# Kernel tuning notes

Hardware: AMD Instinct MI355X
Metric: run time of the kernel (lower is better)

Reference implementation:

```python
import jax, jax.numpy as jnp
import numpy as np

N = 8192      # nodes
NIN = 128     # input feature dim
NH = 128      # hidden dim
NC = 8        # communities
CS = N // NC  # community size


def setup_inputs() -> dict:
    key = jax.random.key(0)
    k = jax.random.split(key, 6)
    seq1 = jax.random.normal(k[0], (1, N, NIN), jnp.float32)
    seq2 = jax.random.normal(k[1], (1, N, NIN), jnp.float32)
    # dense row-stochastic-ish adjacency so GCN activations stay O(1)
    adj = jax.random.uniform(k[2], (1, N, N), jnp.float32) * (2.0 / N)
    cc_label = jnp.arange(N, dtype=jnp.int32).reshape(NC, CS)  # partition of nodes
    W = jax.random.normal(k[3], (NIN, NH), jnp.float32) / np.float32(np.sqrt(NIN))
    b = jnp.zeros((NH,), jnp.float32)
    Wb = jax.random.normal(k[4], (NH, NH), jnp.float32) / np.float32(np.sqrt(NH))
    bb = jnp.zeros((), jnp.float32)
    return {"seq1": seq1, "seq2": seq2, "adj": adj, "cc_label": cc_label,
            "W": W, "b": b, "Wb": Wb, "bb": bb}


def reference(seq1, seq2, adj, cc_label, W, b, Wb, bb):
    def gcn(seq):
        fts = jnp.einsum('bnd,dh->bnh', seq, W)            # linear
        agg = jnp.einsum('bnm,bmh->bnh', adj, fts) + b     # neighborhood aggregation
        return jax.nn.relu(agg)

    h1 = gcn(seq1)[0]   # [N, NH]
    h2 = gcn(seq2)[0]   # [N, NH]

    # ragged per-community gather (communities are equal-size here)
    hg1 = h1[cc_label]  # [NC, CS, NH]
    hg2 = h2[cc_label]  # [NC, CS, NH]

    # AvgReadout (msk=None) + sigmoid -> per-community summary
    c = jax.nn.sigmoid(jnp.mean(hg1, axis=1))              # [NC, NH]

    # Discriminator: bilinear f_k(h, c) = h @ Wb @ c + bb
    cw = jnp.einsum('hk,nk->nh', Wb, c)                    # [NC, NH]
    sc1 = jnp.einsum('nch,nh->nc', hg1, cw) + bb           # [NC, CS]
    sc2 = jnp.einsum('nch,nh->nc', hg2, cw) + bb           # [NC, CS]

    # scalar scatter-back (each node written exactly once)
    flat = cc_label.reshape(-1)
    ret1 = jnp.zeros((N,), h1.dtype).at[flat].set(sc1.reshape(-1))
    ret2 = jnp.zeros((N,), h2.dtype).at[flat].set(sc2.reshape(-1))
    return jnp.concatenate([ret1, ret2])[None, :]          # [1, 2N]
```

## Files before the change

kernel.cpp:

```cpp
#include <hip/hip_runtime.h>


#define NN    8192
#define NCOLS 256
#define ASCALE 4096.0f
#define AINV  (1.0f/4096.0f)

typedef _Float16 half8 __attribute__((ext_vector_type(8)));
typedef float    f32x4 __attribute__((ext_vector_type(4)));

__device__ __forceinline__ void gload16(const void* g, void* l) {
  __builtin_amdgcn_global_load_lds(
      (const __attribute__((address_space(1))) char*)g,
      (__attribute__((address_space(3))) char*)l, 16, 0, 0);
}

__global__ void k0_init(const int* __restrict__ cc, int* __restrict__ node_comm,
                        float* __restrict__ S) {
  int i = blockIdx.x * 256 + threadIdx.x;
  if (i < 1024) S[i] = 0.0f;
  node_comm[cc[i]] = i >> 10;
}

__global__ __launch_bounds__(256) void k1_fts(const float* __restrict__ seq1,
                                              const float* __restrict__ seq2,
                                              const float* __restrict__ W,
                                              _Float16* __restrict__ F) {
  __shared__ char lds[65536];
  _Float16* Wt  = (_Float16*)lds;
  float*    sSeq = (float*)(lds + 32768);
  const int tid = threadIdx.x;
  const int lane = tid & 63;
  const int w = tid >> 6;
  const int l15 = lane & 15;
  const int g = lane >> 4;
  const int m0 = blockIdx.x * 64;

  for (int it = 0; it < 64; ++it) {
    int idx = it * 256 + tid;
    int d = idx >> 7, hc = idx & 127;
    int byte = (hc * 256 + d * 2) ^ ((hc & 7) << 4);
    *(_Float16*)(lds + byte) = (_Float16)W[idx];
  }

  const float* seqp[2] = {seq1, seq2};
  const int srow = tid >> 5;
  const int sck = tid & 31;

  for (int s = 0; s < 2; ++s) {
    __syncthreads();
    const float* sp = seqp[s];
#pragma unroll
    for (int i = 0; i < 8; ++i) {
      int row = i * 8 + srow;
      gload16(sp + (size_t)(m0 + row) * 128 + ((sck ^ (row & 7)) << 2),
              (char*)sSeq + i * 4096 + w * 1024);
    }
    asm volatile("s_waitcnt vmcnt(0)" ::: "memory");
    __syncthreads();

    f32x4 acc[4][2] = {};
    const float4* S4 = (const float4*)sSeq;
    const float4* W4 = (const float4*)Wt;
#pragma unroll
    for (int kk = 0; kk < 4; ++kk) {
      half8 bf[2];
#pragma unroll
      for (int nf = 0; nf < 2; ++nf) {
        int col = w * 32 + nf * 16 + l15;
        float4 bv = W4[(col * 16 + kk * 4 + g) ^ (col & 7)];
        bf[nf] = *(const half8*)&bv;
      }
#pragma unroll
      for (int mf = 0; mf < 4; ++mf) {
        int row = mf * 16 + l15;
        int bidx = row * 32 + kk * 8 + g * 2;
        float4 u = S4[bidx ^ (row & 7)];
        float4 v = S4[(bidx + 1) ^ (row & 7)];
        half8 af;
#pragma unroll
        for (int j = 0; j < 4; ++j) af[j] = (_Float16)(((const float*)&u)[j]);
#pragma unroll
        for (int j = 0; j < 4; ++j) af[4 + j] = (_Float16)(((const float*)&v)[j]);
#pragma unroll
        for (int nf = 0; nf < 2; ++nf)
          acc[mf][nf] = __builtin_amdgcn_mfma_f32_16x16x32_f16(af, bf[nf], acc[mf][nf], 0, 0, 0);
      }
    }
    __syncthreads();
    _Float16* img = (_Float16*)sSeq;
#pragma unroll
    for (int mf = 0; mf < 4; ++mf)
#pragma unroll
      for (int nf = 0; nf < 2; ++nf) {
        int col = w * 32 + nf * 16 + l15;
#pragma unroll
        for (int j = 0; j < 4; ++j) {
          int kl = mf * 16 + g * 4 + j;
          img[(kl >> 5) * 4096 + col * 32 + (kl & 31)] = (_Float16)acc[mf][nf][j];
        }
      }
    __syncthreads();
    const float4* src4 = (const float4*)sSeq;
#pragma unroll
    for (int i = 0; i < 4; ++i) {
      int e = i * 256 + tid;
      int kt = e >> 9, off = e & 511;
      ((float4*)(F + (size_t)(2 * blockIdx.x + kt) * 8192))[s * 512 + off] = src4[e];
    }
  }
}

__global__ __launch_bounds__(512) void k2_gemm(const float* __restrict__ adj,
                                               const _Float16* __restrict__ F,
                                               float* __restrict__ Pp) {
  __shared__ float    sA0[4096];
  __shared__ float    sA1[4096];
  __shared__ _Float16 sB0[8192];
  __shared__ _Float16 sB1[8192];
  const int tid = threadIdx.x;
  const int lane = tid & 63;
  const int w = tid >> 6;
  const int l15 = lane & 15;
  const int g = lane >> 4;
  const int row0 = blockIdx.x * 128;
  const int ks = blockIdx.y;
  const int kcol0 = ks * 2048;

  const int ar0 = tid >> 3;
  const int ac = tid & 7;
  const float* asrc0 = adj + (size_t)(row0 + ar0) * NN + kcol0 + ((ac ^ (ar0 & 7)) << 2);
  const float* asrc1 = adj + (size_t)(row0 + ar0 + 64) * NN + kcol0 + ((ac ^ (ar0 & 7)) << 2);
  const char*  bsrc  = (const char*)F + (size_t)(ks * 64) * 16384 + (size_t)tid * 16;

  auto stage = [&](float* sA, _Float16* sB, int t) {
    gload16(asrc0 + t * 32, (char*)sA + w * 1024);
    gload16(asrc1 + t * 32, (char*)sA + 8192 + w * 1024);
    const char* bs = bsrc + (size_t)t * 16384;
    gload16(bs,        (char*)sB + w * 1024);
    gload16(bs + 8192, (char*)sB + 8192 + w * 1024);
  };

  const int wm = w >> 2, wn = w & 3;
  f32x4 acc[4][4] = {};

  auto compute = [&](const float* sA, const _Float16* sB) {
    const float4* A4 = (const float4*)sA;
    const float4* B4 = (const float4*)sB;
    half8 bf[4];
#pragma unroll
    for (int nf = 0; nf < 4; ++nf) {
      int col = wn * 64 + nf * 16 + l15;
      float4 bv = B4[col * 4 + g];
      bf[nf] = *(const half8*)&bv;
    }
#pragma unroll
    for (int mf = 0; mf < 4; ++mf) {
      int row = wm * 64 + mf * 16 + l15;
      int bidx = row * 8 + g * 2;
      float4 u = A4[bidx ^ (row & 7)];
      float4 v = A4[(bidx + 1) ^ (row & 7)];
      half8 af;
#pragma unroll
      for (int j = 0; j < 4; ++j) af[j] = (_Float16)(((const float*)&u)[j] * ASCALE);
#pragma unroll
      for (int j = 0; j < 4; ++j) af[4 + j] = (_Float16)(((const float*)&v)[j] * ASCALE);
#pragma unroll
      for (int nf = 0; nf < 4; ++nf)
        acc[mf][nf] = __builtin_amdgcn_mfma_f32_16x16x32_f16(af, bf[nf], acc[mf][nf], 0, 0, 0);
    }
  };

  stage(sA0, sB0, 0);
  asm volatile("s_waitcnt vmcnt(0)" ::: "memory");
  __syncthreads();
  for (int t = 0; t < 64; t += 2) {
    stage(sA1, sB1, t + 1);
    compute(sA0, sB0);
    asm volatile("s_waitcnt vmcnt(0)" ::: "memory");
    __syncthreads();
    if (t + 2 < 64) stage(sA0, sB0, t + 2);
    compute(sA1, sB1);
    asm volatile("s_waitcnt vmcnt(0)" ::: "memory");
    __syncthreads();
  }

#pragma unroll
  for (int mf = 0; mf < 4; ++mf)
#pragma unroll
    for (int nf = 0; nf < 4; ++nf) {
      int col = wn * 64 + nf * 16 + l15;
#pragma unroll
      for (int j = 0; j < 4; ++j) {
        int row = row0 + wm * 64 + mf * 16 + g * 4 + j;
        Pp[((size_t)ks * NN + row) * NCOLS + col] = acc[mf][nf][j];
      }
    }
}

__global__ void k2r_reduce(const float* __restrict__ Pp, const float* __restrict__ b,
                           float* __restrict__ h) {
  int gid = blockIdx.x * 256 + threadIdx.x;
  size_t base = (size_t)gid * 4;
  float4 p0 = *(const float4*)(Pp + base);
  float4 p1 = *(const float4*)(Pp + base + 2097152);
  float4 p2 = *(const float4*)(Pp + base + 4194304);
  float4 p3 = *(const float4*)(Pp + base + 6291456);
  int n0 = (int)(base & 255) & 127;
  float4 r;
  r.x = fmaxf((p0.x + p1.x + p2.x + p3.x) * AINV + b[n0],     0.f);
  r.y = fmaxf((p0.y + p1.y + p2.y + p3.y) * AINV + b[n0 + 1], 0.f);
  r.z = fmaxf((p0.z + p1.z + p2.z + p3.z) * AINV + b[n0 + 2], 0.f);
  r.w = fmaxf((p0.w + p1.w + p2.w + p3.w) * AINV + b[n0 + 3], 0.f);
  *(float4*)(h + base) = r;
}

__global__ __launch_bounds__(128) void k3a_csum(const float* __restrict__ h,
                                                const int* __restrict__ node_comm,
                                                float* __restrict__ S) {
  int hh = threadIdx.x;
  int n0 = blockIdx.x * 32;
  float a0=0,a1=0,a2=0,a3=0,a4=0,a5=0,a6=0,a7=0;
  for (int i = 0; i < 32; ++i) {
    int node = n0 + i;
    int c = node_comm[node];
    float v = h[(size_t)node * 256 + hh];
    a0 += (c == 0) ? v : 0.f;  a1 += (c == 1) ? v : 0.f;
    a2 += (c == 2) ? v : 0.f;  a3 += (c == 3) ? v : 0.f;
    a4 += (c == 4) ? v : 0.f;  a5 += (c == 5) ? v : 0.f;
    a6 += (c == 6) ? v : 0.f;  a7 += (c == 7) ? v : 0.f;
  }
  if (a0 != 0.f) atomicAdd(&S[0 * 128 + hh], a0);
  if (a1 != 0.f) atomicAdd(&S[1 * 128 + hh], a1);
  if (a2 != 0.f) atomicAdd(&S[2 * 128 + hh], a2);
  if (a3 != 0.f) atomicAdd(&S[3 * 128 + hh], a3);
  if (a4 != 0.f) atomicAdd(&S[4 * 128 + hh], a4);
  if (a5 != 0.f) atomicAdd(&S[5 * 128 + hh], a5);
  if (a6 != 0.f) atomicAdd(&S[6 * 128 + hh], a6);
  if (a7 != 0.f) atomicAdd(&S[7 * 128 + hh], a7);
}

__global__ __launch_bounds__(128) void k3b_cw(const float* __restrict__ S,
                                              const float* __restrict__ Wb,
                                              float* __restrict__ cw) {
  __shared__ float sc[128];
  int ci = blockIdx.x;
  int hh = threadIdx.x;
  float m = S[ci * 128 + hh] * (1.0f / 1024.0f);
  sc[hh] = 1.0f / (1.0f + __expf(-m));
  __syncthreads();
  const float4* wr = (const float4*)(Wb + (size_t)hh * 128);
  float acc = 0.f;
#pragma unroll 8
  for (int k4 = 0; k4 < 32; ++k4) {
    float4 wv = wr[k4];
    acc += wv.x * sc[k4 * 4 + 0] + wv.y * sc[k4 * 4 + 1]
         + wv.z * sc[k4 * 4 + 2] + wv.w * sc[k4 * 4 + 3];
  }
  cw[ci * 128 + hh] = acc;
}

__global__ __launch_bounds__(256) void k5_score(const float* __restrict__ h,
                                                const int* __restrict__ node_comm,
                                                const float* __restrict__ cw,
                                                const float* __restrict__ bbp,
                                                float* __restrict__ out) {
  int tid = threadIdx.x;
  int q = tid & 15, nl = tid >> 4;
  int node = blockIdx.x * 16 + nl;
  int c = node_comm[node];
  const float* hr = h + (size_t)node * 256;
  const float* cr = cw + c * 128;
  float4 c0 = *(const float4*)(cr + q * 8);
  float4 c1 = *(const float4*)(cr + q * 8 + 4);
  float4 a0 = *(const float4*)(hr + q * 8);
  float4 a1 = *(const float4*)(hr + q * 8 + 4);
  float p1 = a0.x*c0.x + a0.y*c0.y + a0.z*c0.z + a0.w*c0.w
           + a1.x*c1.x + a1.y*c1.y + a1.z*c1.z + a1.w*c1.w;
  float4 b0 = *(const float4*)(hr + 128 + q * 8);
  float4 b1 = *(const float4*)(hr + 128 + q * 8 + 4);
  float p2 = b0.x*c0.x + b0.y*c0.y + b0.z*c0.z + b0.w*c0.w
           + b1.x*c1.x + b1.y*c1.y + b1.z*c1.z + b1.w*c1.w;
#pragma unroll
  for (int m = 8; m >= 1; m >>= 1) {
    p1 += __shfl_xor(p1, m, 64);
    p2 += __shfl_xor(p2, m, 64);
  }
  if (q == 0) {
    float bb = bbp[0];
    out[node] = p1 + bb;
    out[8192 + node] = p2 + bb;
  }
}

extern "C" void kernel_launch(void* const* d_in, const int* in_sizes, int n_in,
                              void* d_out, int out_size, void* d_ws, size_t ws_size,
                              hipStream_t stream) {
  (void)in_sizes; (void)n_in; (void)out_size; (void)ws_size;
  const float* seq1 = (const float*)d_in[0];
  const float* seq2 = (const float*)d_in[1];
  const float* adj  = (const float*)d_in[2];
  const int*   cc   = (const int*)d_in[3];
  const float* W    = (const float*)d_in[4];
  const float* b    = (const float*)d_in[5];
  const float* Wb   = (const float*)d_in[6];
  const float* bb   = (const float*)d_in[7];
  float* out = (float*)d_out;

  char* ws = (char*)d_ws;
  _Float16* F   = (_Float16*)(ws);
  float* h      = (float*)(ws + (4u << 20));
  float* Pp     = (float*)(ws + (12u << 20));
  float* S      = (float*)(ws + (44u << 20));
  float* cw     = (float*)(ws + (44u << 20) + 4096);
  int* node_comm = (int*)(ws + (44u << 20) + 8192);

  k0_init<<<dim3(32), dim3(256), 0, stream>>>(cc, node_comm, S);
  k1_fts<<<dim3(128), dim3(256), 0, stream>>>(seq1, seq2, W, F);
  k2_gemm<<<dim3(64, 4), dim3(512), 0, stream>>>(adj, F, Pp);
  k2r_reduce<<<dim3(2048), dim3(256), 0, stream>>>(Pp, b, h);
  k3a_csum<<<dim3(256), dim3(128), 0, stream>>>(h, node_comm, S);
  k3b_cw<<<dim3(8), dim3(128), 0, stream>>>(S, Wb, cw);
  k5_score<<<dim3(512), dim3(256), 0, stream>>>(h, node_comm, cw, bb, out);
}
```

Measured before the change: 125.7 us.

## Triple-buffer adjacency GEMM loads with partial vmcnt waits

Replaces the double-buffered LDS pipeline in the main aggregation GEMM with a three-stage ring buffer. Loads run two tiles ahead, and each step waits only until the oldest tile has landed (vmcnt(8)) instead of draining all outstanding loads. This keeps more global-to-LDS traffic in flight, hiding memory latency behind the MFMA work. LDS use rises from 64KB to 96KB per block, which may reduce occupancy. It also adds a second barrier per iteration.

```diff
diff --git a/kernel.cpp b/kernel.cpp
--- a/kernel.cpp
+++ b/kernel.cpp
@@ -8,6 +8,8 @@
 
 typedef _Float16 half8 __attribute__((ext_vector_type(8)));
 typedef float    f32x4 __attribute__((ext_vector_type(4)));
+
+#define VMCNT(n) asm volatile("s_waitcnt vmcnt(" #n ")" ::: "memory")
 
 __device__ __forceinline__ void gload16(const void* g, void* l) {
   __builtin_amdgcn_global_load_lds(
@@ -114,10 +116,8 @@
 __global__ __launch_bounds__(512) void k2_gemm(const float* __restrict__ adj,
                                                const _Float16* __restrict__ F,
                                                float* __restrict__ Pp) {
-  __shared__ float    sA0[4096];
-  __shared__ float    sA1[4096];
-  __shared__ _Float16 sB0[8192];
-  __shared__ _Float16 sB1[8192];
+  __shared__ float    sA[3][4096];
+  __shared__ _Float16 sB[3][8192];
   const int tid = threadIdx.x;
   const int lane = tid & 63;
   const int w = tid >> 6;
@@ -133,20 +133,20 @@
   const float* asrc1 = adj + (size_t)(row0 + ar0 + 64) * NN + kcol0 + ((ac ^ (ar0 & 7)) << 2);
   const char*  bsrc  = (const char*)F + (size_t)(ks * 64) * 16384 + (size_t)tid * 16;
 
-  auto stage = [&](float* sA, _Float16* sB, int t) {
-    gload16(asrc0 + t * 32, (char*)sA + w * 1024);
-    gload16(asrc1 + t * 32, (char*)sA + 8192 + w * 1024);
+  auto stage = [&](int buf, int t) {
+    gload16(asrc0 + t * 32, (char*)sA[buf] + w * 1024);
+    gload16(asrc1 + t * 32, (char*)sA[buf] + 8192 + w * 1024);
     const char* bs = bsrc + (size_t)t * 16384;
-    gload16(bs,        (char*)sB + w * 1024);
-    gload16(bs + 8192, (char*)sB + 8192 + w * 1024);
+    gload16(bs,        (char*)sB[buf] + w * 1024);
+    gload16(bs + 8192, (char*)sB[buf] + 8192 + w * 1024);
   };
 
   const int wm = w >> 2, wn = w & 3;
   f32x4 acc[4][4] = {};
 
-  auto compute = [&](const float* sA, const _Float16* sB) {
-    const float4* A4 = (const float4*)sA;
-    const float4* B4 = (const float4*)sB;
+  auto compute = [&](int buf) {
+    const float4* A4 = (const float4*)sA[buf];
+    const float4* B4 = (const float4*)sB[buf];
     half8 bf[4];
 #pragma unroll
     for (int nf = 0; nf < 4; ++nf) {
@@ -171,19 +171,24 @@
     }
   };
 
-  stage(sA0, sB0, 0);
-  asm volatile("s_waitcnt vmcnt(0)" ::: "memory");
-  __syncthreads();
-  for (int t = 0; t < 64; t += 2) {
-    stage(sA1, sB1, t + 1);
-    compute(sA0, sB0);
-    asm volatile("s_waitcnt vmcnt(0)" ::: "memory");
-    __syncthreads();
-    if (t + 2 < 64) stage(sA0, sB0, t + 2);
-    compute(sA1, sB1);
-    asm volatile("s_waitcnt vmcnt(0)" ::: "memory");
-    __syncthreads();
-  }
+  stage(0, 0);
+  stage(1, 1);
+  stage(2, 2);
+  int cur = 0;
+  for (int t = 0; t < 61; ++t) {
+    VMCNT(8);
+    __builtin_amdgcn_s_barrier();
+    compute(cur);
+    __builtin_amdgcn_s_barrier();
+    stage(cur, t + 3);
+    cur = (cur == 2) ? 0 : cur + 1;
+  }
+  VMCNT(8); __builtin_amdgcn_s_barrier();
+  compute(cur); cur = (cur == 2) ? 0 : cur + 1;
+  VMCNT(4); __builtin_amdgcn_s_barrier();
+  compute(cur); cur = (cur == 2) ? 0 : cur + 1;
+  VMCNT(0); __builtin_amdgcn_s_barrier();
+  compute(cur);
 
 #pragma unroll
   for (int mf = 0; mf < 4; ++mf)
```

New measurement: 128.9 us. 2.6% more time.

## Restructure adjacency GEMM to stage fp16 A in LDS and stream B from global

Applied to the files above, without the earlier changes.

The k2_gemm main loop is rewritten. Adjacency tiles are now loaded into registers, converted to fp16 once, and stored into a swizzled fp16 LDS buffer that covers 256 columns per stage. The B operand (F) is read directly from global/L2 into registers with one-step prefetch instead of being staged in LDS. Register-level software pipelining overlaps the next A tile's loads with the MFMAs, and this removes the redundant per-wave fp32-to-fp16 conversion of A along with most barriers. The cost is higher register pressure and more global reads of B per wave, which may raise latency.

```diff
diff --git a/kernel.cpp b/kernel.cpp
--- a/kernel.cpp
+++ b/kernel.cpp
@@ -7,6 +7,7 @@
 #define AINV  (1.0f/4096.0f)
 
 typedef _Float16 half8 __attribute__((ext_vector_type(8)));
+typedef _Float16 half4v __attribute__((ext_vector_type(4)));
 typedef float    f32x4 __attribute__((ext_vector_type(4)));
 
 __device__ __forceinline__ void gload16(const void* g, void* l) {
@@ -114,10 +115,7 @@
 __global__ __launch_bounds__(512) void k2_gemm(const float* __restrict__ adj,
                                                const _Float16* __restrict__ F,
                                                float* __restrict__ Pp) {
-  __shared__ float    sA0[4096];
-  __shared__ float    sA1[4096];
-  __shared__ _Float16 sB0[8192];
-  __shared__ _Float16 sB1[8192];
+  __shared__ __align__(16) _Float16 sA[2][32768];
   const int tid = threadIdx.x;
   const int lane = tid & 63;
   const int w = tid >> 6;
@@ -125,63 +123,85 @@
   const int g = lane >> 4;
   const int row0 = blockIdx.x * 128;
   const int ks = blockIdx.y;
-  const int kcol0 = ks * 2048;
-
-  const int ar0 = tid >> 3;
-  const int ac = tid & 7;
-  const float* asrc0 = adj + (size_t)(row0 + ar0) * NN + kcol0 + ((ac ^ (ar0 & 7)) << 2);
-  const float* asrc1 = adj + (size_t)(row0 + ar0 + 64) * NN + kcol0 + ((ac ^ (ar0 & 7)) << 2);
-  const char*  bsrc  = (const char*)F + (size_t)(ks * 64) * 16384 + (size_t)tid * 16;
-
-  auto stage = [&](float* sA, _Float16* sB, int t) {
-    gload16(asrc0 + t * 32, (char*)sA + w * 1024);
-    gload16(asrc1 + t * 32, (char*)sA + 8192 + w * 1024);
-    const char* bs = bsrc + (size_t)t * 16384;
-    gload16(bs,        (char*)sB + w * 1024);
-    gload16(bs + 8192, (char*)sB + 8192 + w * 1024);
+  const int wm = w >> 2, wn = w & 3;
+
+  const float* abase = adj + (size_t)(row0 + w * 16) * NN + (size_t)ks * 2048 + lane * 4;
+  const _Float16* fbase = F + (size_t)(ks * 64) * 8192;
+
+  f32x4 acc[4][4] = {};
+
+  auto cvt_store = [&](int b, int i, float4 v) {
+    int row = w * 16 + i;
+    char* dst = (char*)sA[b] + row * 512 + ((lane * 8) ^ ((row & 15) << 4));
+    half4v h;
+    h[0] = (_Float16)(v.x * ASCALE); h[1] = (_Float16)(v.y * ASCALE);
+    h[2] = (_Float16)(v.z * ASCALE); h[3] = (_Float16)(v.w * ASCALE);
+    *(half4v*)dst = h;
   };
 
-  const int wm = w >> 2, wn = w & 3;
-  f32x4 acc[4][4] = {};
-
-  auto compute = [&](const float* sA, const _Float16* sB) {
-    const float4* A4 = (const float4*)sA;
-    const float4* B4 = (const float4*)sB;
-    half8 bf[4];
-#pragma unroll
-    for (int nf = 0; nf < 4; ++nf) {
-      int col = wn * 64 + nf * 16 + l15;
-      float4 bv = B4[col * 4 + g];
-      bf[nf] = *(const half8*)&bv;
-    }
-#pragma unroll
-    for (int mf = 0; mf < 4; ++mf) {
-      int row = wm * 64 + mf * 16 + l15;
-      int bidx = row * 8 + g * 2;
-      float4 u = A4[bidx ^ (row & 7)];
-      float4 v = A4[(bidx + 1) ^ (row & 7)];
-      half8 af;
-#pragma unroll
-      for (int j = 0; j < 4; ++j) af[j] = (_Float16)(((const float*)&u)[j] * ASCALE);
-#pragma unroll
-      for (int j = 0; j < 4; ++j) af[4 + j] = (_Float16)(((const float*)&v)[j] * ASCALE);
-#pragma unroll
-      for (int nf = 0; nf < 4; ++nf)
-        acc[mf][nf] = __builtin_amdgcn_mfma_f32_16x16x32_f16(af, bf[nf], acc[mf][nf], 0, 0, 0);
-    }
-  };
-
-  stage(sA0, sB0, 0);
-  asm volatile("s_waitcnt vmcnt(0)" ::: "memory");
+  {
+    float4 pv[16];
+#pragma unroll
+    for (int i = 0; i < 16; ++i) pv[i] = *(const float4*)(abase + (size_t)i * NN);
+#pragma unroll
+    for (int i = 0; i < 16; ++i) cvt_store(0, i, pv[i]);
+  }
   __syncthreads();
-  for (int t = 0; t < 64; t += 2) {
-    stage(sA1, sB1, t + 1);
-    compute(sA0, sB0);
-    asm volatile("s_waitcnt vmcnt(0)" ::: "memory");
-    __syncthreads();
-    if (t + 2 < 64) stage(sA0, sB0, t + 2);
-    compute(sA1, sB1);
-    asm volatile("s_waitcnt vmcnt(0)" ::: "memory");
+
+  int colb[4], rowb[4], rsw[4];
+#pragma unroll
+  for (int nf = 0; nf < 4; ++nf) colb[nf] = (wn * 64 + nf * 16 + l15) * 32 + g * 8;
+#pragma unroll
+  for (int mf = 0; mf < 4; ++mf) {
+    int row = wm * 64 + mf * 16 + l15;
+    rowb[mf] = row * 512; rsw[mf] = (row & 15) << 4;
+  }
+
+  half8 bfc[4], bfn[4];
+#pragma unroll
+  for (int nf = 0; nf < 4; ++nf) {
+    float4 t = *(const float4*)(fbase + colb[nf]);
+    bfc[nf] = *(const half8*)&t;
+  }
+
+  for (int m = 0; m < 8; ++m) {
+    const int b = m & 1;
+    const bool lastm = (m == 7);
+    const char* ab = (const char*)sA[b];
+    const float* anext = abase + (m + 1) * 256;
+    float4 ba[8][2];
+#pragma unroll
+    for (int s = 0; s < 8; ++s) {
+      if (!(lastm && s == 7)) {
+        const _Float16* fb = fbase + (size_t)(m * 8 + s + 1) * 8192;
+#pragma unroll
+        for (int nf = 0; nf < 4; ++nf) {
+          float4 t = *(const float4*)(fb + colb[nf]);
+          bfn[nf] = *(const half8*)&t;
+        }
+      }
+      if (!lastm) {
+        ba[s][0] = *(const float4*)(anext + (size_t)(2 * s) * NN);
+        ba[s][1] = *(const float4*)(anext + (size_t)(2 * s + 1) * NN);
+      }
+#pragma unroll
+      for (int mf = 0; mf < 4; ++mf) {
+        half8 af = *(const half8*)(ab + rowb[mf] + ((s * 64 + g * 16) ^ rsw[mf]));
+#pragma unroll
+        for (int nf = 0; nf < 4; ++nf)
+          acc[mf][nf] = __builtin_amdgcn_mfma_f32_16x16x32_f16(af, bfc[nf], acc[mf][nf], 0, 0, 0);
+      }
+      if (!lastm && s >= 2) {
+        cvt_store(b ^ 1, 2 * (s - 2),     ba[s - 2][0]);
+        cvt_store(b ^ 1, 2 * (s - 2) + 1, ba[s - 2][1]);
+      }
+#pragma unroll
+      for (int nf = 0; nf < 4; ++nf) bfc[nf] = bfn[nf];
+    }
+    if (!lastm) {
+      cvt_store(b ^ 1, 12, ba[6][0]); cvt_store(b ^ 1, 13, ba[6][1]);
+      cvt_store(b ^ 1, 14, ba[7][0]); cvt_store(b ^ 1, 15, ba[7][1]);
+    }
     __syncthreads();
   }
 
```

Result: faster. 119.9 us (-4.6%).

## Fuse adjacency GEMM with bias/ReLU and community sums, drop split-K partials

Applied to the files above, without the earlier changes.

Replaces the split-K adjacency GEMM, its partial-sum reduction and the atomic community-sum kernel with one kernel per 32-row slab that runs the full K range. It converts adj to fp16 while staging into LDS and streams F straight from global memory in registers. The epilogue applies bias and ReLU, writes h, and accumulates per-community partial sums in LDS for a separate small reduce kernel. Node-community init moves into k1, so there are fewer launches and no partial-product round trip through memory. The risk is that only 256 blocks with 32-row tiles re-read all of F from L2 per block, and adj loads use plain global loads rather than async LDS loads.

```diff
diff --git a/kernel.cpp b/kernel.cpp
--- a/kernel.cpp
+++ b/kernel.cpp
@@ -7,6 +7,7 @@
 #define AINV  (1.0f/4096.0f)
 
 typedef _Float16 half8 __attribute__((ext_vector_type(8)));
+typedef _Float16 half4v __attribute__((ext_vector_type(4)));
 typedef float    f32x4 __attribute__((ext_vector_type(4)));
 
 __device__ __forceinline__ void gload16(const void* g, void* l) {
@@ -15,17 +16,12 @@
       (__attribute__((address_space(3))) char*)l, 16, 0, 0);
 }
 
-__global__ void k0_init(const int* __restrict__ cc, int* __restrict__ node_comm,
-                        float* __restrict__ S) {
-  int i = blockIdx.x * 256 + threadIdx.x;
-  if (i < 1024) S[i] = 0.0f;
-  node_comm[cc[i]] = i >> 10;
-}
-
 __global__ __launch_bounds__(256) void k1_fts(const float* __restrict__ seq1,
                                               const float* __restrict__ seq2,
                                               const float* __restrict__ W,
-                                              _Float16* __restrict__ F) {
+                                              _Float16* __restrict__ F,
+                                              const int* __restrict__ cc,
+                                              int* __restrict__ node_comm) {
   __shared__ char lds[65536];
   _Float16* Wt  = (_Float16*)lds;
   float*    sSeq = (float*)(lds + 32768);
@@ -36,6 +32,11 @@
   const int g = lane >> 4;
   const int m0 = blockIdx.x * 64;
 
+  if (tid < 64) {
+    int i = blockIdx.x * 64 + tid;
+    node_comm[cc[i]] = i >> 10;
+  }
+
   for (int it = 0; it < 64; ++it) {
     int idx = it * 256 + tid;
     int d = idx >> 7, hc = idx & 127;
@@ -111,153 +112,138 @@
   }
 }
 
-__global__ __launch_bounds__(512) void k2_gemm(const float* __restrict__ adj,
-                                               const _Float16* __restrict__ F,
-                                               float* __restrict__ Pp) {
-  __shared__ float    sA0[4096];
-  __shared__ float    sA1[4096];
-  __shared__ _Float16 sB0[8192];
-  __shared__ _Float16 sB1[8192];
+__global__ __launch_bounds__(512) void k2_big(const float* __restrict__ adj,
+                                              const _Float16* __restrict__ F,
+                                              const float* __restrict__ bias,
+                                              const int* __restrict__ node_comm,
+                                              float* __restrict__ h,
+                                              float* __restrict__ pB) {
+  __shared__ __align__(16) _Float16 sA[2][16384];
+  __shared__ float sP[1024];
+  __shared__ int   sNC[32];
   const int tid = threadIdx.x;
   const int lane = tid & 63;
-  const int w = tid >> 6;
+  const int w8 = tid >> 6;
   const int l15 = lane & 15;
   const int g = lane >> 4;
-  const int row0 = blockIdx.x * 128;
-  const int ks = blockIdx.y;
-  const int kcol0 = ks * 2048;
-
-  const int ar0 = tid >> 3;
-  const int ac = tid & 7;
-  const float* asrc0 = adj + (size_t)(row0 + ar0) * NN + kcol0 + ((ac ^ (ar0 & 7)) << 2);
-  const float* asrc1 = adj + (size_t)(row0 + ar0 + 64) * NN + kcol0 + ((ac ^ (ar0 & 7)) << 2);
-  const char*  bsrc  = (const char*)F + (size_t)(ks * 64) * 16384 + (size_t)tid * 16;
-
-  auto stage = [&](float* sA, _Float16* sB, int t) {
-    gload16(asrc0 + t * 32, (char*)sA + w * 1024);
-    gload16(asrc1 + t * 32, (char*)sA + 8192 + w * 1024);
-    const char* bs = bsrc + (size_t)t * 16384;
-    gload16(bs,        (char*)sB + w * 1024);
-    gload16(bs + 8192, (char*)sB + 8192 + w * 1024);
+  const int b = blockIdx.x;
+  const float* aslab = adj + (size_t)b * 32 * NN;
+
+  if (tid < 32) sNC[tid] = node_comm[b * 32 + tid];
+  sP[tid] = 0.0f; sP[tid + 512] = 0.0f;
+
+  const int srow4 = tid >> 7;
+  const int sc4 = tid & 127;
+
+  auto stg_write = [&](int buf, int row, int c4, float4 v) {
+    char* dst = (char*)sA[buf] + row * 1024 + ((c4 * 8) ^ ((row & 7) << 4));
+    half4v hv;
+    hv[0] = (_Float16)(v.x * ASCALE); hv[1] = (_Float16)(v.y * ASCALE);
+    hv[2] = (_Float16)(v.z * ASCALE); hv[3] = (_Float16)(v.w * ASCALE);
+    *(half4v*)dst = hv;
   };
 
-  const int wm = w >> 2, wn = w & 3;
-  f32x4 acc[4][4] = {};
-
-  auto compute = [&](const float* sA, const _Float16* sB) {
-    const float4* A4 = (const float4*)sA;
-    const float4* B4 = (const float4*)sB;
-    half8 bf[4];
-#pragma unroll
-    for (int nf = 0; nf < 4; ++nf) {
-      int col = wn * 64 + nf * 16 + l15;
-      float4 bv = B4[col * 4 + g];
-      bf[nf] = *(const half8*)&bv;
-    }
-#pragma unroll
-    for (int mf = 0; mf < 4; ++mf) {
-      int row = wm * 64 + mf * 16 + l15;
-      int bidx = row * 8 + g * 2;
-      float4 u = A4[bidx ^ (row & 7)];
-      float4 v = A4[(bidx + 1) ^ (row & 7)];
-      half8 af;
-#pragma unroll
-      for (int j = 0; j < 4; ++j) af[j] = (_Float16)(((const float*)&u)[j] * ASCALE);
-#pragma unroll
-      for (int j = 0; j < 4; ++j) af[4 + j] = (_Float16)(((const float*)&v)[j] * ASCALE);
-#pragma unroll
-      for (int nf = 0; nf < 4; ++nf)
-        acc[mf][nf] = __builtin_amdgcn_mfma_f32_16x16x32_f16(af, bf[nf], acc[mf][nf], 0, 0, 0);
-    }
-  };
-
-  stage(sA0, sB0, 0);
-  asm volatile("s_waitcnt vmcnt(0)" ::: "memory");
+  {
+    float4 pv[8];
+#pragma unroll
+    for (int it = 0; it < 8; ++it)
+      pv[it] = *(const float4*)(aslab + (size_t)(it * 4 + srow4) * NN + sc4 * 4);
+#pragma unroll
+    for (int it = 0; it < 8; ++it)
+      stg_write(0, it * 4 + srow4, sc4, pv[it]);
+  }
+
+  const int colb0 = (w8 * 32 + l15) * 32 + g * 8;
+  const int colb1 = (w8 * 32 + 16 + l15) * 32 + g * 8;
+  f32x4 acc[2][2] = {};
+  half8 bfc0, bfc1, bfn0, bfn1;
+  {
+    float4 t0 = *(const float4*)(F + colb0);
+    float4 t1 = *(const float4*)(F + colb1);
+    bfc0 = *(const half8*)&t0; bfc1 = *(const half8*)&t1;
+  }
   __syncthreads();
-  for (int t = 0; t < 64; t += 2) {
-    stage(sA1, sB1, t + 1);
-    compute(sA0, sB0);
-    asm volatile("s_waitcnt vmcnt(0)" ::: "memory");
-    __syncthreads();
-    if (t + 2 < 64) stage(sA0, sB0, t + 2);
-    compute(sA1, sB1);
-    asm volatile("s_waitcnt vmcnt(0)" ::: "memory");
-    __syncthreads();
-  }
-
-#pragma unroll
-  for (int mf = 0; mf < 4; ++mf)
-#pragma unroll
-    for (int nf = 0; nf < 4; ++nf) {
-      int col = wn * 64 + nf * 16 + l15;
-#pragma unroll
-      for (int j = 0; j < 4; ++j) {
-        int row = row0 + wm * 64 + mf * 16 + g * 4 + j;
-        Pp[((size_t)ks * NN + row) * NCOLS + col] = acc[mf][nf][j];
-      }
-    }
-}
-
-__global__ void k2r_reduce(const float* __restrict__ Pp, const float* __restrict__ b,
-                           float* __restrict__ h) {
-  int gid = blockIdx.x * 256 + threadIdx.x;
-  size_t base = (size_t)gid * 4;
-  float4 p0 = *(const float4*)(Pp + base);
-  float4 p1 = *(const float4*)(Pp + base + 2097152);
-  float4 p2 = *(const float4*)(Pp + base + 4194304);
-  float4 p3 = *(const float4*)(Pp + base + 6291456);
-  int n0 = (int)(base & 255) & 127;
-  float4 r;
-  r.x = fmaxf((p0.x + p1.x + p2.x + p3.x) * AINV + b[n0],     0.f);
-  r.y = fmaxf((p0.y + p1.y + p2.y + p3.y) * AINV + b[n0 + 1], 0.f);
-  r.z = fmaxf((p0.z + p1.z + p2.z + p3.z) * AINV + b[n0 + 2], 0.f);
-  r.w = fmaxf((p0.w + p1.w + p2.w + p3.w) * AINV + b[n0 + 3], 0.f);
-  *(float4*)(h + base) = r;
-}
-
-__global__ __launch_bounds__(128) void k3a_csum(const float* __restrict__ h,
-                                                const int* __restrict__ node_comm,
-                                                float* __restrict__ S) {
-  int hh = threadIdx.x;
-  int n0 = blockIdx.x * 32;
-  float a0=0,a1=0,a2=0,a3=0,a4=0,a5=0,a6=0,a7=0;
-  for (int i = 0; i < 32; ++i) {
-    int node = n0 + i;
-    int c = node_comm[node];
-    float v = h[(size_t)node * 256 + hh];
-    a0 += (c == 0) ? v : 0.f;  a1 += (c == 1) ? v : 0.f;
-    a2 += (c == 2) ? v : 0.f;  a3 += (c == 3) ? v : 0.f;
-    a4 += (c == 4) ? v : 0.f;  a5 += (c == 5) ? v : 0.f;
-    a6 += (c == 6) ? v : 0.f;  a7 += (c == 7) ? v : 0.f;
-  }
-  if (a0 != 0.f) atomicAdd(&S[0 * 128 + hh], a0);
-  if (a1 != 0.f) atomicAdd(&S[1 * 128 + hh], a1);
-  if (a2 != 0.f) atomicAdd(&S[2 * 128 + hh], a2);
-  if (a3 != 0.f) atomicAdd(&S[3 * 128 + hh], a3);
-  if (a4 != 0.f) atomicAdd(&S[4 * 128 + hh], a4);
-  if (a5 != 0.f) atomicAdd(&S[5 * 128 + hh], a5);
-  if (a6 != 0.f) atomicAdd(&S[6 * 128 + hh], a6);
-  if (a7 != 0.f) atomicAdd(&S[7 * 128 + hh], a7);
-}
-
-__global__ __launch_bounds__(128) void k3b_cw(const float* __restrict__ S,
-                                              const float* __restrict__ Wb,
-                                              float* __restrict__ cw) {
-  __shared__ float sc[128];
-  int ci = blockIdx.x;
-  int hh = threadIdx.x;
-  float m = S[ci * 128 + hh] * (1.0f / 1024.0f);
-  sc[hh] = 1.0f / (1.0f + __expf(-m));
+
+  float4 av[8];
+  for (int w = 0; w < 16; ++w) {
+    const int buf = w & 1;
+    const char* ab = (const char*)sA[buf];
+    const float* anext = aslab + (size_t)(w + 1) * 512 + sc4 * 4;
+#pragma unroll
+    for (int s = 0; s < 16; ++s) {
+      const int msub = w * 16 + s;
+      if (!(w == 15 && s == 15)) {
+        const _Float16* fb = F + (size_t)(msub + 1) * 8192;
+        float4 t0 = *(const float4*)(fb + colb0);
+        float4 t1 = *(const float4*)(fb + colb1);
+        bfn0 = *(const half8*)&t0; bfn1 = *(const half8*)&t1;
+      }
+      if (w < 15) {
+        if (s < 4) {
+          av[2 * s]     = *(const float4*)(anext + (size_t)(2 * s * 4 + srow4) * NN);
+          av[2 * s + 1] = *(const float4*)(anext + (size_t)((2 * s + 1) * 4 + srow4) * NN);
+        }
+        if (s >= 8) {
+          int it = s - 8;
+          stg_write(buf ^ 1, it * 4 + srow4, sc4, av[it]);
+        }
+      }
+#pragma unroll
+      for (int mf = 0; mf < 2; ++mf) {
+        int row = mf * 16 + l15;
+        half8 af = *(const half8*)(ab + row * 1024 + ((s * 64 + g * 16) ^ ((row & 7) << 4)));
+        acc[mf][0] = __builtin_amdgcn_mfma_f32_16x16x32_f16(af, bfc0, acc[mf][0], 0, 0, 0);
+        acc[mf][1] = __builtin_amdgcn_mfma_f32_16x16x32_f16(af, bfc1, acc[mf][1], 0, 0, 0);
+      }
+      bfc0 = bfn0; bfc1 = bfn1;
+    }
+    __syncthreads();
+  }
+
+  const int col0 = w8 * 32 + l15, col1 = w8 * 32 + 16 + l15;
+  const float bl0 = bias[col0 & 127], bl1 = bias[col1 & 127];
+#pragma unroll
+  for (int mf = 0; mf < 2; ++mf)
+#pragma unroll
+    for (int j = 0; j < 4; ++j) {
+      int row = mf * 16 + g * 4 + j;
+      int node = b * 32 + row;
+      float v0 = fmaxf(acc[mf][0][j] * AINV + bl0, 0.f);
+      float v1 = fmaxf(acc[mf][1][j] * AINV + bl1, 0.f);
+      h[(size_t)node * 256 + col0] = v0;
+      h[(size_t)node * 256 + col1] = v1;
+      if (w8 < 4) {
+        int c = sNC[row];
+        atomicAdd(&sP[c * 128 + col0], v0);
+        atomicAdd(&sP[c * 128 + col1], v1);
+      }
+    }
   __syncthreads();
-  const float4* wr = (const float4*)(Wb + (size_t)hh * 128);
-  float acc = 0.f;
+  pB[(size_t)b * 1024 + tid] = sP[tid];
+  pB[(size_t)b * 1024 + 512 + tid] = sP[tid + 512];
+}
+
+__global__ __launch_bounds__(128) void k3_cw(const float* __restrict__ pB,
+                                             const float* __restrict__ Wb,
+                                             float* __restrict__ cw) {
+  __shared__ float sig[128];
+  const int ci = blockIdx.x;
+  const int d = threadIdx.x;
+  float s = 0.f;
+#pragma unroll 8
+  for (int b = 0; b < 256; ++b)
+    s += pB[(size_t)b * 1024 + ci * 128 + d];
+  sig[d] = 1.0f / (1.0f + __expf(-s * (1.0f / 1024.0f)));
+  __syncthreads();
+  const float4* wr = (const float4*)(Wb + (size_t)d * 128);
+  const float4* s4 = (const float4*)sig;
+  float a = 0.f;
 #pragma unroll 8
   for (int k4 = 0; k4 < 32; ++k4) {
-    float4 wv = wr[k4];
-    acc += wv.x * sc[k4 * 4 + 0] + wv.y * sc[k4 * 4 + 1]
-         + wv.z * sc[k4 * 4 + 2] + wv.w * sc[k4 * 4 + 3];
-  }
-  cw[ci * 128 + hh] = acc;
+    float4 wv = wr[k4], sv = s4[k4];
+    a += wv.x * sv.x + wv.y * sv.y + wv.z * sv.z + wv.w * sv.w;
+  }
+  cw[ci * 128 + d] = a;
 }
 
 __global__ __launch_bounds__(256) void k5_score(const float* __restrict__ h,
@@ -308,18 +294,14 @@
   float* out = (float*)d_out;
 
   char* ws = (char*)d_ws;
-  _Float16* F   = (_Float16*)(ws);
-  float* h      = (float*)(ws + (4u << 20));
-  float* Pp     = (float*)(ws + (12u << 20));
-  float* S      = (float*)(ws + (44u << 20));
-  float* cw     = (float*)(ws + (44u << 20) + 4096);
-  int* node_comm = (int*)(ws + (44u << 20) + 8192);
-
-  k0_init<<<dim3(32), dim3(256), 0, stream>>>(cc, node_comm, S);
-  k1_fts<<<dim3(128), dim3(256), 0, stream>>>(seq1, seq2, W, F);
-  k2_gemm<<<dim3(64, 4), dim3(512), 0, stream>>>(adj, F, Pp);
-  k2r_reduce<<<dim3(2048), dim3(256), 0, stream>>>(Pp, b, h);
-  k3a_csum<<<dim3(256), dim3(128), 0, stream>>>(h, node_comm, S);
-  k3b_cw<<<dim3(8), dim3(128), 0, stream>>>(S, Wb, cw);
+  _Float16* F    = (_Float16*)(ws);
+  float* h       = (float*)(ws + (4u << 20));
+  float* pB      = (float*)(ws + (12u << 20));
+  float* cw      = (float*)(ws + (13u << 20));
+  int* node_comm = (int*)(ws + (13u << 20) + 4096);
+
+  k1_fts<<<dim3(128), dim3(256), 0, stream>>>(seq1, seq2, W, F, cc, node_comm);
+  k2_big<<<dim3(256), dim3(512), 0, stream>>>(adj, F, b, node_comm, h, pB);
+  k3_cw<<<dim3(8), dim3(128), 0, stream>>>(pB, Wb, cw);
   k5_score<<<dim3(512), dim3(256), 0, stream>>>(h, node_comm, cw, bb, out);
 }
```

New measurement: 145.9 us. 1.16x slower.
